# Kernel optimization log

Hardware: AMD Instinct MI355X
Metric: run time of the kernel (lower is better)

Reference implementation:

```python
import jax, jax.numpy as jnp
import numpy as np

NUM_HEADS = 32
NUM_KV_HEADS = 8
HEAD_DIM = 128
ROPE_THETA = 10000.0


def _rope_cos_sin(seq_len, head_dim, dtype):
    inv_freq = 1.0 / (ROPE_THETA ** (jnp.arange(0, head_dim, 2, dtype=jnp.float32) / head_dim))
    t = jnp.arange(seq_len, dtype=jnp.float32)
    freqs = jnp.outer(t, inv_freq)              # [S, hd/2]
    emb = jnp.concatenate([freqs, freqs], axis=-1)  # [S, hd]
    return jnp.cos(emb).astype(dtype), jnp.sin(emb).astype(dtype)


def _rotate_half(x):
    h = x.shape[-1] // 2
    return jnp.concatenate([-x[..., h:], x[..., :h]], axis=-1)


def _apply_rope(x, cos, sin):
    # x: [B, H, S, D]; cos/sin: [S, D] (position_ids = arange(S) in prefill)
    return x * cos[None, None] + _rotate_half(x) * sin[None, None]


def setup_inputs() -> dict:
    key = jax.random.key(0)
    ks = jax.random.split(key, 5)
    B, S, H = 1, 2048, 4096
    return {
        "hidden_states": jax.random.normal(ks[0], (B, S, H), dtype=jnp.float32),
        "Wq": jax.random.normal(ks[1], (H, NUM_HEADS * HEAD_DIM), dtype=jnp.float32) * 0.02,
        "Wk": jax.random.normal(ks[2], (H, NUM_KV_HEADS * HEAD_DIM), dtype=jnp.float32) * 0.02,
        "Wv": jax.random.normal(ks[3], (H, NUM_KV_HEADS * HEAD_DIM), dtype=jnp.float32) * 0.02,
        "Wo": jax.random.normal(ks[4], (NUM_HEADS * HEAD_DIM, H), dtype=jnp.float32) * 0.02,
    }


def reference(hidden_states, Wq, Wk, Wv, Wo):
    B, S, H = hidden_states.shape
    nh, nkv, hd = NUM_HEADS, NUM_KV_HEADS, HEAD_DIM
    groups = nh // nkv

    # fused QKV projections (bias-free, Llama-style)
    q = (hidden_states @ Wq).reshape(B, S, nh, hd).transpose(0, 2, 1, 3)   # [B,nh,S,D]
    k = (hidden_states @ Wk).reshape(B, S, nkv, hd).transpose(0, 2, 1, 3)  # [B,nkv,S,D]
    v = (hidden_states @ Wv).reshape(B, S, nkv, hd).transpose(0, 2, 1, 3)

    # inline RoPE on q and k
    cos, sin = _rope_cos_sin(S, hd, q.dtype)
    q = _apply_rope(q, cos, sin)
    k = _apply_rope(k, cos, sin)

    # GQA: repeat kv heads to match query heads (num_key_value_groups)
    k = jnp.repeat(k, groups, axis=1)  # [B,nh,S,D]
    v = jnp.repeat(v, groups, axis=1)

    scale = 1.0 / jnp.sqrt(jnp.asarray(hd, dtype=q.dtype))
    logits = jnp.einsum("bhqd,bhkd->bhqk", q, k) * scale  # [B,nh,S,S]

    # prefill causal mask (phys_past_len = 0)
    causal = jnp.tril(jnp.ones((S, S), dtype=bool))
    neg = jnp.asarray(jnp.finfo(logits.dtype).min, dtype=logits.dtype)
    logits = jnp.where(causal[None, None], logits, neg)

    attn = jax.nn.softmax(logits.astype(jnp.float32), axis=-1).astype(q.dtype)
    out = jnp.einsum("bhqk,bhkd->bhqd", attn, v)           # [B,nh,S,D]
    out = out.transpose(0, 2, 1, 3).reshape(B, S, nh * hd)  # [B,S,H]
    return out @ Wo
```

## Files before the change

kernel.cpp:

```cpp
#include <hip/hip_runtime.h>
#include <cstdint>
#include <cstddef>

typedef __attribute__((ext_vector_type(4))) float f32x4;
typedef __attribute__((ext_vector_type(16))) float f32x16;
typedef __attribute__((ext_vector_type(8))) short bf16x8;
typedef __attribute__((ext_vector_type(2))) unsigned int u32x2;

#define S_LEN   2048
#define HID     4096
#define NH      32
#define NKV     8
#define HD      128
#define QKV_N   6144

typedef const __attribute__((address_space(1))) unsigned int* gptr_t;
typedef __attribute__((address_space(3))) unsigned int* lptr_t;

__device__ __forceinline__ void gload_lds16(const void* g, void* l) {
  __builtin_amdgcn_global_load_lds((gptr_t)g, (lptr_t)l, 16, 0, 0);
}

__device__ __forceinline__ ushort f2bf(float f) {
  union { float f; uint32_t u; } v; v.f = f;
  uint32_t r = v.u + 0x7FFFu + ((v.u >> 16) & 1u);
  return (ushort)(r >> 16);
}
__device__ __forceinline__ float bf2f(ushort u) {
  union { uint32_t u; float f; } v; v.u = ((uint32_t)u) << 16;
  return v.f;
}

__global__ void cast_f32_bf16(const float* __restrict__ in, ushort* __restrict__ out, int n) {
  int i = (blockIdx.x * 256 + threadIdx.x) * 4;
  if (i >= n) return;
  float4 v = *reinterpret_cast<const float4*>(in + i);
  ushort4 o;
  o.x = f2bf(v.x); o.y = f2bf(v.y); o.z = f2bf(v.z); o.w = f2bf(v.w);
  *reinterpret_cast<ushort4*>(out + i) = o;
}

__global__ void transpose_cast(const float* __restrict__ in, ushort* __restrict__ out, int R, int C) {
  __shared__ float t[32][33];
  int tx = threadIdx.x & 31, ty = threadIdx.x >> 5;
  int r0 = blockIdx.y * 32, c0 = blockIdx.x * 32;
#pragma unroll
  for (int i = 0; i < 32; i += 8)
    t[ty + i][tx] = in[(size_t)(r0 + ty + i) * C + c0 + tx];
  __syncthreads();
#pragma unroll
  for (int i = 0; i < 32; i += 8)
    out[(size_t)(c0 + ty + i) * R + r0 + tx] = f2bf(t[tx][ty + i]);
}

template <bool BF16_OUT>
__global__ __launch_bounds__(256, 2) void gemm_bt(
    const ushort* __restrict__ A, const ushort* __restrict__ B,
    void* __restrict__ Cp, int M, int N, int K) {
  __shared__ ushort a_lds[128 * 32];
  __shared__ ushort b_lds[128 * 32];
  const int tid = threadIdx.x;
  const int wid = tid >> 6, lane = tid & 63;
  const int l16 = lane & 15, lk = lane >> 4;
  const int wr = wid >> 1, wc = wid & 1;
  const size_t a_row0 = (size_t)blockIdx.y * 128;
  const size_t b_row0 = (size_t)blockIdx.x * 128;

  f32x4 acc[4][4] = {};

  for (int kt = 0; kt < K; kt += 32) {
    __syncthreads();
#pragma unroll
    for (int i = 0; i < 2; ++i) {
      int c = i * 256 + wid * 64 + lane;
      int row = c >> 2, cc = c & 3;
      gload_lds16(A + (a_row0 + row) * K + kt + cc * 8, &a_lds[c * 8]);
      gload_lds16(B + (b_row0 + row) * K + kt + cc * 8, &b_lds[c * 8]);
    }
    __syncthreads();

    bf16x8 af[4], bf[4];
#pragma unroll
    for (int m = 0; m < 4; ++m)
      af[m] = *reinterpret_cast<const bf16x8*>(&a_lds[(wr * 64 + m * 16 + l16) * 32 + lk * 8]);
#pragma unroll
    for (int n = 0; n < 4; ++n)
      bf[n] = *reinterpret_cast<const bf16x8*>(&b_lds[(wc * 64 + n * 16 + l16) * 32 + lk * 8]);
#pragma unroll
    for (int m = 0; m < 4; ++m)
#pragma unroll
      for (int n = 0; n < 4; ++n)
        acc[m][n] = __builtin_amdgcn_mfma_f32_16x16x32_bf16(af[m], bf[n], acc[m][n], 0, 0, 0);
  }

#pragma unroll
  for (int m = 0; m < 4; ++m) {
    int row_b = wr * 64 + m * 16 + lk * 4;
#pragma unroll
    for (int n = 0; n < 4; ++n) {
      int col = (int)b_row0 + wc * 64 + n * 16 + l16;
#pragma unroll
      for (int r = 0; r < 4; ++r) {
        size_t row = a_row0 + row_b + r;
        if constexpr (BF16_OUT)
          ((ushort*)Cp)[row * N + col] = f2bf(acc[m][n][r]);
        else
          ((float*)Cp)[row * N + col] = acc[m][n][r];
      }
    }
  }
}

__global__ void rope_kernel(ushort* __restrict__ QKV) {
  int idx = blockIdx.x * 256 + threadIdx.x;
  int dg = idx & 7;
  int t = idx >> 3;
  int s = t / 40;
  int hh = t - s * 40;
  if (s >= S_LEN) return;
  int col = (hh < NH) ? hh * HD : HID + (hh - NH) * HD;
  ushort* base = QKV + (size_t)s * QKV_N + col + dg * 8;

  union U { uint4 v; ushort u[8]; };
  U L, H, OL, OH;
  L.v = *reinterpret_cast<const uint4*>(base);
  H.v = *reinterpret_cast<const uint4*>(base + 64);
  const float C0 = 13.287712379549449f / 64.0f;
#pragma unroll
  for (int j = 0; j < 8; ++j) {
    int d = dg * 8 + j;
    float invf = exp2f(-(float)d * C0);
    float ang = (float)s * invf;
    float sn, cs;
    sincosf(ang, &sn, &cs);
    float xl = bf2f(L.u[j]), xh = bf2f(H.u[j]);
    OL.u[j] = f2bf(xl * cs - xh * sn);
    OH.u[j] = f2bf(xh * cs + xl * sn);
  }
  *reinterpret_cast<uint4*>(base) = OL.v;
  *reinterpret_cast<uint4*>(base + 64) = OH.v;
}

__global__ void transpose_v(const ushort* __restrict__ QKV, ushort* __restrict__ Vt) {
  __shared__ ushort t[64][65];
  int s0 = blockIdx.x * 64;
  int d0 = blockIdx.y * 64;
  int hkv = blockIdx.z;
  int tx = threadIdx.x & 63, ty = threadIdx.x >> 6;
#pragma unroll
  for (int i = 0; i < 64; i += 4)
    t[i + ty][tx] = QKV[(size_t)(s0 + i + ty) * QKV_N + HID + NKV * HD + hkv * HD + d0 + tx];
  __syncthreads();
#pragma unroll
  for (int i = 0; i < 64; i += 4)
    Vt[((size_t)hkv * HD + d0 + i + ty) * S_LEN + s0 + tx] = t[tx][i + ty];
}

__global__ __launch_bounds__(256, 2) void attn_kernel(
    const ushort* __restrict__ QKV, const ushort* __restrict__ Vt, ushort* __restrict__ AO) {
  constexpr float SCALE = 0.08838834764831845f;
  __shared__ ushort k_lds[2][64 * 128];
  __shared__ ushort v_lds[2][128 * 64];

  const int qb = blockIdx.x;
  const int h = blockIdx.y;
  const int hkv = h >> 2;
  const int q0 = qb * 128;
  const int tid = threadIdx.x, wid = tid >> 6, lane = tid & 63;
  const int l32 = lane & 31;
  const int hi = lane >> 5;
  const int qg = q0 + wid * 32 + l32;

  bf16x8 qf[8];
  {
    const ushort* qrow = QKV + (size_t)qg * QKV_N + h * HD + hi * 8;
#pragma unroll
    for (int ds = 0; ds < 8; ++ds)
      qf[ds] = *reinterpret_cast<const bf16x8*>(qrow + ds * 16);
  }

  float m_run = -1e30f, l_run = 0.f;
  f32x16 oacc[4] = {};

  auto stageKV = [&](int buf, int kt) {
#pragma unroll
    for (int i = 0; i < 4; ++i) {
      int c = i * 256 + wid * 64 + lane;
      int row = c >> 4, ch = c & 15;
      int sch = ch ^ (row & 7);
      gload_lds16(QKV + (size_t)(kt * 64 + row) * QKV_N + HID + hkv * HD + sch * 8,
                  &k_lds[buf][c * 8]);
    }
#pragma unroll
    for (int i = 0; i < 4; ++i) {
      int c = i * 256 + wid * 64 + lane;
      int row = c >> 3, ch = c & 7;
      int sch = ch ^ (row & 7);
      gload_lds16(Vt + ((size_t)hkv * HD + row) * S_LEN + (size_t)kt * 64 + sch * 8,
                  &v_lds[buf][c * 8]);
    }
  };

  stageKV(0, 0);
  __syncthreads();

  const int nt = 2 * qb + 2;
  for (int kt = 0; kt < nt; ++kt) {
    const int cur = kt & 1;
    if (kt + 1 < nt) stageKV(cur ^ 1, kt + 1);

    if (kt * 64 <= q0 + wid * 32 + 31) {
      float p[32];
      __builtin_amdgcn_s_setprio(1);
#pragma unroll
      for (int kf = 0; kf < 2; ++kf) {
        f32x16 s = {};
        int rk = kf * 32 + l32;
#pragma unroll
        for (int ds = 0; ds < 8; ++ds) {
          int c16 = (ds * 2 + hi) ^ (rk & 7);
          bf16x8 kfr = *reinterpret_cast<const bf16x8*>(&k_lds[cur][rk * 128 + c16 * 8]);
          s = __builtin_amdgcn_mfma_f32_32x32x16_bf16(kfr, qf[ds], s, 0, 0, 0);
        }
#pragma unroll
        for (int r = 0; r < 16; ++r) p[kf * 16 + r] = s[r] * SCALE;
      }
      __builtin_amdgcn_s_setprio(0);

      if (kt * 64 + 63 > q0 + wid * 32) {
#pragma unroll
        for (int kf = 0; kf < 2; ++kf)
#pragma unroll
          for (int r = 0; r < 16; ++r) {
            int kl = kf * 32 + (r & 3) + 8 * (r >> 2) + 4 * hi;
            if (kt * 64 + kl > qg) p[kf * 16 + r] = -1e30f;
          }
      }

      float mt = p[0];
#pragma unroll
      for (int i = 1; i < 32; ++i) mt = fmaxf(mt, p[i]);
      mt = fmaxf(mt, __shfl_xor(mt, 32, 64));
      float mn = fmaxf(m_run, mt);
      float alpha = __expf(m_run - mn);
      float ls = 0.f;
#pragma unroll
      for (int i = 0; i < 32; ++i) { p[i] = __expf(p[i] - mn); ls += p[i]; }
      ls += __shfl_xor(ls, 32, 64);
      l_run = l_run * alpha + ls;
      m_run = mn;
#pragma unroll
      for (int f = 0; f < 4; ++f)
#pragma unroll
        for (int r = 0; r < 16; ++r) oacc[f][r] *= alpha;

      union PW { uint32_t w[4]; bf16x8 v; } pa[4];
#pragma unroll
      for (int ks = 0; ks < 4; ++ks) {
        uint32_t x0, x1, y0, y1;
        asm("v_cvt_pk_bf16_f32 %0, %1, %2" : "=v"(x0) : "v"(p[8 * ks + 0]), "v"(p[8 * ks + 1]));
        asm("v_cvt_pk_bf16_f32 %0, %1, %2" : "=v"(x1) : "v"(p[8 * ks + 2]), "v"(p[8 * ks + 3]));
        asm("v_cvt_pk_bf16_f32 %0, %1, %2" : "=v"(y0) : "v"(p[8 * ks + 4]), "v"(p[8 * ks + 5]));
        asm("v_cvt_pk_bf16_f32 %0, %1, %2" : "=v"(y1) : "v"(p[8 * ks + 6]), "v"(p[8 * ks + 7]));
        u32x2 r0 = __builtin_amdgcn_permlane32_swap(x0, y0, false, false);
        u32x2 r1 = __builtin_amdgcn_permlane32_swap(x1, y1, false, false);
        pa[ks].w[0] = r0.x; pa[ks].w[1] = r1.x; pa[ks].w[2] = r0.y; pa[ks].w[3] = r1.y;
      }

      __builtin_amdgcn_s_setprio(1);
#pragma unroll
      for (int ks = 0; ks < 4; ++ks) {
#pragma unroll
        for (int f = 0; f < 4; ++f) {
          int dv = f * 32 + l32;
          int c8 = (2 * ks + hi) ^ (dv & 7);
          bf16x8 vfr = *reinterpret_cast<const bf16x8*>(&v_lds[cur][dv * 64 + c8 * 8]);
          oacc[f] = __builtin_amdgcn_mfma_f32_32x32x16_bf16(vfr, pa[ks].v, oacc[f], 0, 0, 0);
        }
      }
      __builtin_amdgcn_s_setprio(0);
    }

    __syncthreads();
  }

  float inv_l = 1.0f / l_run;
  ushort* aorow = AO + (size_t)qg * HID + h * HD;
#pragma unroll
  for (int f = 0; f < 4; ++f)
#pragma unroll
    for (int g = 0; g < 4; ++g) {
      ushort4 o;
      o.x = f2bf(oacc[f][g * 4 + 0] * inv_l);
      o.y = f2bf(oacc[f][g * 4 + 1] * inv_l);
      o.z = f2bf(oacc[f][g * 4 + 2] * inv_l);
      o.w = f2bf(oacc[f][g * 4 + 3] * inv_l);
      *reinterpret_cast<ushort4*>(aorow + f * 32 + g * 8 + 4 * hi) = o;
    }
}

extern "C" void kernel_launch(void* const* d_in, const int* in_sizes, int n_in,
                              void* d_out, int out_size, void* d_ws, size_t ws_size,
                              hipStream_t stream) {
  (void)in_sizes; (void)n_in; (void)out_size;
  const float* hs = (const float*)d_in[0];
  const float* Wq = (const float*)d_in[1];
  const float* Wk = (const float*)d_in[2];
  const float* Wv = (const float*)d_in[3];
  const float* Wo = (const float*)d_in[4];
  float* out = (float*)d_out;

  char* ws = (char*)d_ws;
  const size_t OFF_HSB   = 0;
  const size_t OFF_WQKVT = OFF_HSB + 16777216;
  const size_t OFF_WOT   = OFF_WQKVT + 50331648;
  const size_t OFF_QKV   = OFF_WOT + 33554432;
  const size_t OFF_VT    = OFF_QKV + 25165824;
  const size_t OFF_AO    = OFF_VT + 4194304;
  if (ws_size < OFF_AO + 16777216) return;

  ushort* hsb   = (ushort*)(ws + OFF_HSB);
  ushort* WqkvT = (ushort*)(ws + OFF_WQKVT);
  ushort* WoT   = (ushort*)(ws + OFF_WOT);
  ushort* QKV   = (ushort*)(ws + OFF_QKV);
  ushort* Vt    = (ushort*)(ws + OFF_VT);
  ushort* AO    = (ushort*)(ws + OFF_AO);

  cast_f32_bf16<<<8192, 256, 0, stream>>>(hs, hsb, S_LEN * HID);
  transpose_cast<<<dim3(4096 / 32, 4096 / 32), 256, 0, stream>>>(Wq, WqkvT, HID, 4096);
  transpose_cast<<<dim3(1024 / 32, 4096 / 32), 256, 0, stream>>>(Wk, WqkvT + (size_t)4096 * HID, HID, 1024);
  transpose_cast<<<dim3(1024 / 32, 4096 / 32), 256, 0, stream>>>(Wv, WqkvT + (size_t)5120 * HID, HID, 1024);
  transpose_cast<<<dim3(4096 / 32, 4096 / 32), 256, 0, stream>>>(Wo, WoT, 4096, HID);

  gemm_bt<true><<<dim3(QKV_N / 128, S_LEN / 128), 256, 0, stream>>>(hsb, WqkvT, QKV, S_LEN, QKV_N, HID);
  rope_kernel<<<(S_LEN * 40 * 8) / 256, 256, 0, stream>>>(QKV);
  transpose_v<<<dim3(S_LEN / 64, HD / 64, NKV), 256, 0, stream>>>(QKV, Vt);
  attn_kernel<<<dim3(S_LEN / 128, NH), 256, 0, stream>>>(QKV, Vt, AO);
  gemm_bt<false><<<dim3(HID / 128, S_LEN / 128), 256, 0, stream>>>(AO, WoT, out, S_LEN, HID, HID);
}
```

Measured before the change: 369.3 us.

## Rewrite GEMMs with 8-wave double-buffered LDS pipeline, swizzle, XCD remap

Replaces the simple 128x128 single-buffered GEMM with an 8-wave kernel that uses larger tiles (256x256 for QKV, 128x256 for the output projection) and a K-step of 64. Global-to-LDS loads are double-buffered so the next tile is fetched during compute. LDS rows are XOR-swizzled to avoid bank conflicts, and workgroup IDs are remapped so neighbouring tiles land on the same XCD. MFMA phases are interleaved with barriers and s_setprio. Larger tiles and double buffers raise LDS and register pressure, and the output-projection grid shrinks to 256 blocks.

```diff
diff --git a/kernel.cpp b/kernel.cpp
--- a/kernel.cpp
+++ b/kernel.cpp
@@ -53,59 +53,150 @@
     out[(size_t)(c0 + ty + i) * R + r0 + tx] = f2bf(t[tx][ty + i]);
 }
 
-template <bool BF16_OUT>
-__global__ __launch_bounds__(256, 2) void gemm_bt(
+template <int BM, bool BF16_OUT>
+__global__ __launch_bounds__(512, 2) void gemm_bt8(
     const ushort* __restrict__ A, const ushort* __restrict__ B,
-    void* __restrict__ Cp, int M, int N, int K) {
-  __shared__ ushort a_lds[128 * 32];
-  __shared__ ushort b_lds[128 * 32];
+    void* __restrict__ Cp, int N, int K) {
+  constexpr int MR = BM / 32;
+  __shared__ ushort a_lds[2][BM * 64];
+  __shared__ ushort b_lds[2][256 * 64];
   const int tid = threadIdx.x;
   const int wid = tid >> 6, lane = tid & 63;
   const int l16 = lane & 15, lk = lane >> 4;
-  const int wr = wid >> 1, wc = wid & 1;
-  const size_t a_row0 = (size_t)blockIdx.y * 128;
-  const size_t b_row0 = (size_t)blockIdx.x * 128;
-
-  f32x4 acc[4][4] = {};
-
-  for (int kt = 0; kt < K; kt += 32) {
-    __syncthreads();
-#pragma unroll
-    for (int i = 0; i < 2; ++i) {
-      int c = i * 256 + wid * 64 + lane;
-      int row = c >> 2, cc = c & 3;
-      gload_lds16(A + (a_row0 + row) * K + kt + cc * 8, &a_lds[c * 8]);
-      gload_lds16(B + (b_row0 + row) * K + kt + cc * 8, &b_lds[c * 8]);
-    }
-    __syncthreads();
-
-    bf16x8 af[4], bf[4];
-#pragma unroll
-    for (int m = 0; m < 4; ++m)
-      af[m] = *reinterpret_cast<const bf16x8*>(&a_lds[(wr * 64 + m * 16 + l16) * 32 + lk * 8]);
-#pragma unroll
-    for (int n = 0; n < 4; ++n)
-      bf[n] = *reinterpret_cast<const bf16x8*>(&b_lds[(wc * 64 + n * 16 + l16) * 32 + lk * 8]);
-#pragma unroll
-    for (int m = 0; m < 4; ++m)
-#pragma unroll
-      for (int n = 0; n < 4; ++n)
-        acc[m][n] = __builtin_amdgcn_mfma_f32_16x16x32_bf16(af[m], bf[n], acc[m][n], 0, 0, 0);
+  const int wr = wid >> 2, wc = wid & 3;
+
+  const int gx = gridDim.x;
+  const int nwg = gx * gridDim.y;
+  const int orig = blockIdx.y * gx + blockIdx.x;
+  const int q = nwg >> 3, rm = nwg & 7;
+  const int xcd = orig & 7, idx = orig >> 3;
+  const int wgid = (xcd < rm ? xcd * (q + 1) : rm * (q + 1) + (xcd - rm) * q) + idx;
+  const size_t a_row0 = (size_t)(wgid / gx) * BM;
+  const size_t b_row0 = (size_t)(wgid % gx) * 256;
+
+  f32x4 acc[MR][4] = {};
+  const int NT = K >> 6;
+
+  auto stage = [&](int buf, int t) {
+    const size_t kb = (size_t)t << 6;
+#pragma unroll
+    for (int i = 0; i < BM / 64; ++i) {
+      int c = i * 512 + tid;
+      int row = c >> 3, ch = c & 7, sch = ch ^ (row & 7);
+      gload_lds16(A + (a_row0 + row) * K + kb + sch * 8, &a_lds[buf][c * 8]);
+    }
+#pragma unroll
+    for (int i = 0; i < 4; ++i) {
+      int c = i * 512 + tid;
+      int row = c >> 3, ch = c & 7, sch = ch ^ (row & 7);
+      gload_lds16(B + (b_row0 + row) * K + kb + sch * 8, &b_lds[buf][c * 8]);
+    }
+  };
+
+  stage(0, 0);
+  asm volatile("s_waitcnt vmcnt(0)" ::: "memory");
+  __builtin_amdgcn_s_barrier();
+
+  for (int t = 0; t < NT; ++t) {
+    const int cur = t & 1;
+    if (t + 1 < NT) stage(cur ^ 1, t + 1);
+
+    bf16x8 a0[MR / 2][2], a1[MR / 2][2], b0[2][2], b1[2][2];
+#pragma unroll
+    for (int m = 0; m < MR / 2; ++m)
+#pragma unroll
+      for (int kk = 0; kk < 2; ++kk) {
+        int row = wr * (BM / 2) + m * 16 + l16;
+        int c = (kk * 4 + lk) ^ (row & 7);
+        a0[m][kk] = *reinterpret_cast<const bf16x8*>(&a_lds[cur][row * 64 + c * 8]);
+      }
+#pragma unroll
+    for (int n = 0; n < 2; ++n)
+#pragma unroll
+      for (int kk = 0; kk < 2; ++kk) {
+        int row = wc * 64 + n * 16 + l16;
+        int c = (kk * 4 + lk) ^ (row & 7);
+        b0[n][kk] = *reinterpret_cast<const bf16x8*>(&b_lds[cur][row * 64 + c * 8]);
+      }
+    __builtin_amdgcn_s_barrier();
+    __builtin_amdgcn_s_setprio(1);
+#pragma unroll
+    for (int m = 0; m < MR / 2; ++m)
+#pragma unroll
+      for (int n = 0; n < 2; ++n)
+#pragma unroll
+        for (int kk = 0; kk < 2; ++kk)
+          acc[m][n] = __builtin_amdgcn_mfma_f32_16x16x32_bf16(a0[m][kk], b0[n][kk], acc[m][n], 0, 0, 0);
+    __builtin_amdgcn_s_setprio(0);
+    __builtin_amdgcn_s_barrier();
+
+#pragma unroll
+    for (int m = 0; m < MR / 2; ++m)
+#pragma unroll
+      for (int kk = 0; kk < 2; ++kk) {
+        int row = wr * (BM / 2) + BM / 4 + m * 16 + l16;
+        int c = (kk * 4 + lk) ^ (row & 7);
+        a1[m][kk] = *reinterpret_cast<const bf16x8*>(&a_lds[cur][row * 64 + c * 8]);
+      }
+    __builtin_amdgcn_s_barrier();
+    __builtin_amdgcn_s_setprio(1);
+#pragma unroll
+    for (int m = 0; m < MR / 2; ++m)
+#pragma unroll
+      for (int n = 0; n < 2; ++n)
+#pragma unroll
+        for (int kk = 0; kk < 2; ++kk)
+          acc[MR / 2 + m][n] = __builtin_amdgcn_mfma_f32_16x16x32_bf16(a1[m][kk], b0[n][kk], acc[MR / 2 + m][n], 0, 0, 0);
+    __builtin_amdgcn_s_setprio(0);
+    __builtin_amdgcn_s_barrier();
+
+#pragma unroll
+    for (int n = 0; n < 2; ++n)
+#pragma unroll
+      for (int kk = 0; kk < 2; ++kk) {
+        int row = wc * 64 + 32 + n * 16 + l16;
+        int c = (kk * 4 + lk) ^ (row & 7);
+        b1[n][kk] = *reinterpret_cast<const bf16x8*>(&b_lds[cur][row * 64 + c * 8]);
+      }
+    __builtin_amdgcn_s_barrier();
+    __builtin_amdgcn_s_setprio(1);
+#pragma unroll
+    for (int m = 0; m < MR / 2; ++m)
+#pragma unroll
+      for (int n = 0; n < 2; ++n)
+#pragma unroll
+        for (int kk = 0; kk < 2; ++kk)
+          acc[m][2 + n] = __builtin_amdgcn_mfma_f32_16x16x32_bf16(a0[m][kk], b1[n][kk], acc[m][2 + n], 0, 0, 0);
+    __builtin_amdgcn_s_setprio(0);
+    __builtin_amdgcn_s_barrier();
+
+    __builtin_amdgcn_s_setprio(1);
+#pragma unroll
+    for (int m = 0; m < MR / 2; ++m)
+#pragma unroll
+      for (int n = 0; n < 2; ++n)
+#pragma unroll
+        for (int kk = 0; kk < 2; ++kk)
+          acc[MR / 2 + m][2 + n] = __builtin_amdgcn_mfma_f32_16x16x32_bf16(a1[m][kk], b1[n][kk], acc[MR / 2 + m][2 + n], 0, 0, 0);
+    __builtin_amdgcn_s_setprio(0);
+
+    asm volatile("s_waitcnt vmcnt(0)" ::: "memory");
+    __builtin_amdgcn_s_barrier();
   }
 
 #pragma unroll
-  for (int m = 0; m < 4; ++m) {
-    int row_b = wr * 64 + m * 16 + lk * 4;
+  for (int m = 0; m < MR; ++m) {
+    const int roff = (m < MR / 2) ? m * 16 : BM / 4 + (m - MR / 2) * 16;
+    size_t row_b = a_row0 + wr * (BM / 2) + roff + lk * 4;
 #pragma unroll
     for (int n = 0; n < 4; ++n) {
       int col = (int)b_row0 + wc * 64 + n * 16 + l16;
 #pragma unroll
       for (int r = 0; r < 4; ++r) {
-        size_t row = a_row0 + row_b + r;
         if constexpr (BF16_OUT)
-          ((ushort*)Cp)[row * N + col] = f2bf(acc[m][n][r]);
+          ((ushort*)Cp)[(row_b + r) * N + col] = f2bf(acc[m][n][r]);
         else
-          ((float*)Cp)[row * N + col] = acc[m][n][r];
+          ((float*)Cp)[(row_b + r) * N + col] = acc[m][n][r];
       }
     }
   }
@@ -332,9 +423,9 @@
   transpose_cast<<<dim3(1024 / 32, 4096 / 32), 256, 0, stream>>>(Wv, WqkvT + (size_t)5120 * HID, HID, 1024);
   transpose_cast<<<dim3(4096 / 32, 4096 / 32), 256, 0, stream>>>(Wo, WoT, 4096, HID);
 
-  gemm_bt<true><<<dim3(QKV_N / 128, S_LEN / 128), 256, 0, stream>>>(hsb, WqkvT, QKV, S_LEN, QKV_N, HID);
+  gemm_bt8<256, true><<<dim3(QKV_N / 256, S_LEN / 256), 512, 0, stream>>>(hsb, WqkvT, QKV, QKV_N, HID);
   rope_kernel<<<(S_LEN * 40 * 8) / 256, 256, 0, stream>>>(QKV);
   transpose_v<<<dim3(S_LEN / 64, HD / 64, NKV), 256, 0, stream>>>(QKV, Vt);
   attn_kernel<<<dim3(S_LEN / 128, NH), 256, 0, stream>>>(QKV, Vt, AO);
-  gemm_bt<false><<<dim3(HID / 128, S_LEN / 128), 256, 0, stream>>>(AO, WoT, out, S_LEN, HID, HID);
-}
+  gemm_bt8<128, false><<<dim3(HID / 256, S_LEN / 128), 512, 0, stream>>>(AO, WoT, out, HID, HID);
+}
```

After: 403.0 us. 1.09x slower.
